# Optimization experiments

Hardware: AMD Instinct MI355X
Metric: run time of the kernel (lower is better)

Reference implementation:

```python
import jax, jax.numpy as jnp
import numpy as np
from jax.scipy.linalg import cho_solve

N = 4096        # num nodes
D = 256         # in_dim == out_dim
NUM_HOPS = 2
R = 32          # subspace_dim
ETA = 0.5
EPS_SUB = 0.5   # eps in coeff = r / (n * eps^2)
LN_EPS = 1e-5


def setup_inputs() -> dict:
    rng = np.random.default_rng(0)
    K = NUM_HOPS + 1
    # sparse-ish binary adjacency mask with self loops
    mask = (rng.random((N, N)) < 0.002).astype(np.float32)
    mask = np.maximum(mask, np.eye(N, dtype=np.float32))
    deg = mask.sum(axis=1, keepdims=True)
    A = (mask / deg).astype(np.float32)          # row-stochastic propagation
    L = (np.eye(N, dtype=np.float32) - A)        # normalized Laplacian
    H = rng.standard_normal((N, D)).astype(np.float32)
    # orthonormal subspace bases per hop, as in __init__ (QR of randn)
    U = np.stack([np.linalg.qr(rng.standard_normal((D, R)))[0][:, :R] for _ in range(K)]).astype(np.float32)
    lambda_laps = np.full((K,), 0.1, dtype=np.float32)
    hop_weights = np.full((K,), 1.0 / K, dtype=np.float32)
    threshold = np.full((D,), 0.05, dtype=np.float32)
    gamma = np.ones((D,), dtype=np.float32)
    beta = np.zeros((D,), dtype=np.float32)
    return {
        "H": jnp.asarray(H), "A": jnp.asarray(A), "adj_mask": jnp.asarray(mask),
        "L": jnp.asarray(L), "U": jnp.asarray(U),
        "lambda_laps": jnp.asarray(lambda_laps), "hop_weights": jnp.asarray(hop_weights),
        "threshold": jnp.asarray(threshold), "gamma": jnp.asarray(gamma), "beta": jnp.asarray(beta),
    }


def reference(H, A, adj_mask, L, U, lambda_laps, hop_weights, threshold, gamma, beta):
    n, d = H.shape
    r = U.shape[-1]
    # multi-hop propagation
    hops = [H]
    Hk = H
    for _ in range(NUM_HOPS):
        Hk = A @ Hk
        hops.append(Hk)
    w = jax.nn.softmax(hop_weights)
    laps = jax.nn.softplus(lambda_laps)
    coeff = r / (n * EPS_SUB ** 2)
    neg = (1.0 - adj_mask) * -1e9
    I_r = jnp.eye(r, dtype=H.dtype)
    agg = jnp.zeros_like(H)        # accumulates grad_k.T, shape [n, d]
    lap_total = jnp.zeros_like(H)
    for k, H_k in enumerate(hops):
        Uk = U[k]                  # [d, r]
        Zk = Uk.T @ H_k.T          # [r, n]
        M = I_r + coeff * (Zk @ Zk.T)              # [r, r], SPD
        Lc = jnp.linalg.cholesky(M)
        M_inv = cho_solve((Lc, True), I_r)         # cholesky_inverse
        MZ = M_inv @ Zk                            # [r, n]
        scores = Zk.T @ MZ + neg                   # [n, n] masked subspace attention
        alpha = jax.nn.softmax(scores, axis=1)
        grad_k = (Uk @ (MZ @ alpha.T)).T           # [n, d]
        agg = agg + w[k] * grad_k
        lap_total = lap_total + laps[k] * (L @ H_k)
    H_half = H + ETA * agg - ETA * lap_total
    # soft-threshold (proj is None since in_dim == out_dim)
    H_out = jnp.sign(H_half) * jax.nn.relu(jnp.abs(H_half) - threshold[None, :])
    H_out = H_out + H              # residual
    mu = H_out.mean(axis=-1, keepdims=True)
    var = H_out.var(axis=-1, keepdims=True)
    H_out = (H_out - mu) / jnp.sqrt(var + LN_EPS) * gamma + beta
    # orthogonality loss over all (k, l) pairs
    K = U.shape[0]
    orth_loss = jnp.asarray(0.0, dtype=H.dtype)
    for k in range(K):
        for l in range(k, K):
            G = U[k].T @ U[l]
            orth_loss = orth_loss + jnp.sum(((G - I_r) if l == k else G) ** 2)
    lap_smooth = jnp.sum(H_out * (L @ H_out))  # trace(H^T L H)
    return H_out, orth_loss, lap_smooth, jax.lax.stop_gradient(w)
```

## Files before the change

### kernel.cpp

```cpp
#include <hip/hip_runtime.h>
#include <math.h>

#define NN 4096
#define DD 256
#define KK 3
#define RR 32
#define MAXNNZ 128

static constexpr float ETA    = 0.5f;
static constexpr float COEFF  = 0.03125f;
static constexpr float LN_EPSF = 1e-5f;

#define OFF_H1   0
#define OFF_H2   (NN*DD)
#define OFF_H3   (2*NN*DD)
#define OFF_Y    (3*NN*DD)
#define OFF_P    (OFF_Y + KK*NN*RR)
#define OFF_M    (OFF_P + KK*NN*RR)
#define OFF_MINV (OFF_M + KK*RR*RR)
#define OFF_SCAL (OFF_MINV + KK*RR*RR)
#define OFF_NNZ  (OFF_SCAL + 8)
#define OFF_COLS (OFF_NNZ + NN)
#define OFF_VALS (OFF_COLS + NN*MAXNNZ)
#define OFF_PART (OFF_VALS + NN*MAXNNZ)
#define OFF_ORTH (OFF_PART + NN/4)
#define OFF_W    (OFF_ORTH + 8)

__global__ void k_csr_prep(const float* __restrict__ A, int* __restrict__ nnz,
                           int* __restrict__ cols, float* __restrict__ vals,
                           const float* __restrict__ hw, const float* __restrict__ ll,
                           const float* __restrict__ U,
                           float* __restrict__ ws, float* __restrict__ out) {
  int b = blockIdx.x;
  int t = threadIdx.x;
  if (b >= NN/4) {
    int p = b - NN/4;
    if (p == 6) {
      if (t == 0) {
        float m = fmaxf(fmaxf(hw[0], hw[1]), hw[2]);
        float e0 = expf(hw[0]-m), e1 = expf(hw[1]-m), e2 = expf(hw[2]-m);
        float s = e0 + e1 + e2;
        float w0 = e0/s, w1 = e1/s, w2 = e2/s;
        ws[OFF_SCAL+0] = w0; ws[OFF_SCAL+1] = w1; ws[OFF_SCAL+2] = w2;
        for (int k = 0; k < KK; ++k) {
          float x = ll[k];
          ws[OFF_SCAL+3+k] = (x > 20.f) ? x : log1pf(expf(x));
        }
        out[NN*DD + 2] = w0; out[NN*DD + 3] = w1; out[NN*DD + 4] = w2;
      }
      for (int idx = t; idx < KK*RR*RR; idx += 256) {
        int rr2 = idx % (RR*RR);
        ws[OFF_M + idx] = ((rr2 / RR) == (rr2 % RR)) ? 1.f : 0.f;
      }
      return;
    }
    int k = (p < 3) ? 0 : ((p < 5) ? 1 : 2);
    int l = (p < 3) ? p : ((p < 5) ? p - 2 : 2);
    int a0 = t >> 5, bb = t & 31;
    float s0 = 0.f, s1 = 0.f, s2 = 0.f, s3 = 0.f;
    for (int dd = 0; dd < DD; ++dd) {
      float ul = U[(size_t)l*DD*RR + dd*RR + bb];
      const float* uk = U + (size_t)k*DD*RR + dd*RR;
      s0 += uk[a0]      * ul;
      s1 += uk[a0 + 8]  * ul;
      s2 += uk[a0 + 16] * ul;
      s3 += uk[a0 + 24] * ul;
    }
    if (k == l && bb == a0)      s0 -= 1.f;
    if (k == l && bb == a0 + 8)  s1 -= 1.f;
    if (k == l && bb == a0 + 16) s2 -= 1.f;
    if (k == l && bb == a0 + 24) s3 -= 1.f;
    float sq = s0*s0 + s1*s1 + s2*s2 + s3*s3;
    #pragma unroll
    for (int o = 32; o > 0; o >>= 1) sq += __shfl_xor(sq, o, 64);
    __shared__ float red[4];
    if ((t & 63) == 0) red[t >> 6] = sq;
    __syncthreads();
    if (t == 0) ws[OFF_ORTH + p] = red[0] + red[1] + red[2] + red[3];
    return;
  }
  int w = t >> 6, lane = t & 63;
  int i = b * 4 + w;
  const float4* row4 = (const float4*)(A + (size_t)i * NN);
  float4 vv[16];
  #pragma unroll
  for (int it = 0; it < 16; ++it) vv[it] = row4[it*64 + lane];
  int* ci = cols + i*MAXNNZ;
  float* vi = vals + i*MAXNNZ;
  unsigned long long lower = lane ? (~0ull >> (64 - lane)) : 0ull;
  int base = 0;
  #pragma unroll
  for (int it = 0; it < 16; ++it) {
    float4 v = vv[it];
    int jb = (it*64 + lane) * 4;
    unsigned long long mx = __ballot(v.x != 0.f);
    unsigned long long my = __ballot(v.y != 0.f);
    unsigned long long mz = __ballot(v.z != 0.f);
    unsigned long long mw = __ballot(v.w != 0.f);
    int before = __popcll(mx & lower) + __popcll(my & lower)
               + __popcll(mz & lower) + __popcll(mw & lower);
    int p0 = base + before;
    int bx = (mx >> lane) & 1, by = (my >> lane) & 1, bz = (mz >> lane) & 1;
    if (v.x != 0.f && p0 < MAXNNZ)                    { ci[p0] = jb;   vi[p0] = v.x; }
    int p1 = p0 + bx;
    if (v.y != 0.f && p1 < MAXNNZ)                    { ci[p1] = jb+1; vi[p1] = v.y; }
    int p2 = p1 + by;
    if (v.z != 0.f && p2 < MAXNNZ)                    { ci[p2] = jb+2; vi[p2] = v.z; }
    int p3 = p2 + bz;
    if (v.w != 0.f && p3 < MAXNNZ)                    { ci[p3] = jb+3; vi[p3] = v.w; }
    base += __popcll(mx) + __popcll(my) + __popcll(mz) + __popcll(mw);
  }
  int n = base < MAXNNZ ? base : MAXNNZ;
  int npad = (n + 7) & ~7;
  for (int e = n + lane; e < npad; e += 64) {
    ci[e] = i;
    vi[e] = 0.f;
  }
  if (lane == 0) nnz[i] = n;
}

__device__ __forceinline__ void spmv_quad(const float* __restrict__ X, int row, int lane,
                                          const int* __restrict__ nnz,
                                          const int* __restrict__ cols,
                                          const float* __restrict__ vals,
                                          float4& acc, float4& own) {
  int d4 = lane * 4;
  int n = nnz[row];
  int npad = (n + 7) & ~7;
  const int* ci = cols + row*MAXNNZ;
  const float* vi = vals + row*MAXNNZ;
  for (int e0 = 0; e0 < npad; e0 += 8) {
    int4 c0 = *(const int4*)(ci + e0);
    int4 c1 = *(const int4*)(ci + e0 + 4);
    float4 v0 = *(const float4*)(vi + e0);
    float4 v1 = *(const float4*)(vi + e0 + 4);
    float4 x0 = *(const float4*)(X + (size_t)c0.x*DD + d4);
    float4 x1 = *(const float4*)(X + (size_t)c0.y*DD + d4);
    float4 x2 = *(const float4*)(X + (size_t)c0.z*DD + d4);
    float4 x3 = *(const float4*)(X + (size_t)c0.w*DD + d4);
    float4 x4 = *(const float4*)(X + (size_t)c1.x*DD + d4);
    float4 x5 = *(const float4*)(X + (size_t)c1.y*DD + d4);
    float4 x6 = *(const float4*)(X + (size_t)c1.z*DD + d4);
    float4 x7 = *(const float4*)(X + (size_t)c1.w*DD + d4);
    if (c0.x == row) own = x0;
    if (c0.y == row) own = x1;
    if (c0.z == row) own = x2;
    if (c0.w == row) own = x3;
    if (c1.x == row) own = x4;
    if (c1.y == row) own = x5;
    if (c1.z == row) own = x6;
    if (c1.w == row) own = x7;
    acc.x += v0.x*x0.x + v0.y*x1.x + v0.z*x2.x + v0.w*x3.x + v1.x*x4.x + v1.y*x5.x + v1.z*x6.x + v1.w*x7.x;
    acc.y += v0.x*x0.y + v0.y*x1.y + v0.z*x2.y + v0.w*x3.y + v1.x*x4.y + v1.y*x5.y + v1.z*x6.y + v1.w*x7.y;
    acc.z += v0.x*x0.z + v0.y*x1.z + v0.z*x2.z + v0.w*x3.z + v1.x*x4.z + v1.y*x5.z + v1.z*x6.z + v1.w*x7.z;
    acc.w += v0.x*x0.w + v0.y*x1.w + v0.z*x2.w + v0.w*x3.w + v1.x*x4.w + v1.y*x5.w + v1.z*x6.w + v1.w*x7.w;
  }
}

__global__ void k_spmvy(const float* __restrict__ X, float* __restrict__ Hout,
                        const int* __restrict__ nnz, const int* __restrict__ cols,
                        const float* __restrict__ vals,
                        const float* __restrict__ Uo, float* __restrict__ Yo,
                        const float* __restrict__ Un, float* __restrict__ Yn) {
  int t = threadIdx.x;
  int r = t >> 6, lane = t & 63;
  int row = blockIdx.x * 4 + r;
  int d4 = lane * 4;
  float4 acc = {0.f, 0.f, 0.f, 0.f};
  float4 own = {0.f, 0.f, 0.f, 0.f};
  spmv_quad(X, row, lane, nnz, cols, vals, acc, own);
  *(float4*)(Hout + (size_t)row*DD + d4) = acc;
  if (!Uo && !Un) return;
  __shared__ float Hs[4][2][DD];
  *(float4*)&Hs[r][0][d4] = own;
  *(float4*)&Hs[r][1][d4] = acc;
  __syncthreads();
  int c = lane & 31, h = lane >> 5;
  if (Uo) {
    float part = 0.f;
    #pragma unroll 8
    for (int d = h*128; d < h*128 + 128; ++d) part += Hs[r][0][d] * Uo[d*RR + c];
    part += __shfl_xor(part, 32, 64);
    if (h == 0) Yo[(size_t)row*RR + c] = part;
  }
  if (Un) {
    float part = 0.f;
    #pragma unroll 8
    for (int d = h*128; d < h*128 + 128; ++d) part += Hs[r][1][d] * Un[d*RR + c];
    part += __shfl_xor(part, 32, 64);
    if (h == 0) Yn[(size_t)row*RR + c] = part;
  }
}

__global__ __launch_bounds__(1024) void k_gram(const float* __restrict__ Y, float* __restrict__ M) {
  int k = blockIdx.y;
  __shared__ float Ys[128*RR];
  int t = threadIdx.x;
  const float* Yk = Y + (size_t)k*NN*RR + (size_t)blockIdx.x*128*RR;
  for (int idx = t; idx < 128*RR; idx += 1024) Ys[idx] = Yk[idx];
  __syncthreads();
  int a = t >> 5, b = t & 31;
  float s = 0.f;
  for (int i = 0; i < 128; ++i) s += Ys[i*RR + a] * Ys[i*RR + b];
  atomicAdd(&M[k*RR*RR + a*RR + b], COEFF * s);
}

__global__ __launch_bounds__(256) void k_gj(const float* __restrict__ M, float* __restrict__ Minv,
                                            const float* __restrict__ U, float* __restrict__ W) {
  int k = blockIdx.x;
  int g = blockIdx.y;
  int t = threadIdx.x;
  __shared__ float B[RR][2*RR + 1];
  for (int idx = t; idx < RR*2*RR; idx += 256) {
    int r = idx >> 6, c = idx & 63;
    B[r][c] = (c < RR) ? M[k*RR*RR + r*RR + c] : ((c - RR == r) ? 1.f : 0.f);
  }
  __syncthreads();
  if (t < 64) {
    for (int p = 0; p < RR; ++p) {
      float rd = 1.f / B[p][p];
      float pb = B[p][t] * rd;
      float f[RR];
      #pragma unroll
      for (int r = 0; r < RR; ++r) f[r] = B[r][p];
      B[p][t] = pb;
      #pragma unroll
      for (int r = 0; r < RR; ++r) {
        if (r == p) continue;
        B[r][t] -= f[r] * pb;
      }
    }
  }
  __syncthreads();
  if (g == 0)
    for (int idx = t; idx < RR*RR; idx += 256)
      Minv[k*RR*RR + idx] = B[idx >> 5][RR + (idx & 31)];
  for (int e = 0; e < 8; ++e) {
    int idx = t + e*256;
    int d = g*64 + (idx >> 5), rr2 = idx & 31;
    const float* ud = U + (size_t)k*DD*RR + (size_t)d*RR;
    float s = 0.f;
    #pragma unroll
    for (int a = 0; a < RR; ++a) s += ud[a] * B[a][RR + rr2];
    W[(size_t)k*DD*RR + (size_t)d*RR + rr2] = s;
  }
}

__global__ __launch_bounds__(256) void k_attn(const float* __restrict__ Y, const float* __restrict__ Minv,
                       float* __restrict__ P, const int* __restrict__ nnz,
                       const int* __restrict__ cols, const float* __restrict__ vals,
                       const float* __restrict__ H2, float* __restrict__ H3) {
  int k = blockIdx.y;
  int t = threadIdx.x;
  int w = t >> 6, lane = t & 63;
  if (blockIdx.x >= NN/4) {
    if (k != 0) return;
    int row = (blockIdx.x - NN/4) * 4 + w;
    float4 acc = {0.f, 0.f, 0.f, 0.f};
    float4 own;
    spmv_quad(H2, row, lane, nnz, cols, vals, acc, own);
    *(float4*)(H3 + (size_t)row*DD + lane*4) = acc;
    return;
  }
  int i = blockIdx.x * 4 + w;
  const float* Yk = Y + (size_t)k*NN*RR;
  __shared__ float Mi[RR*RR];
  __shared__ float Yi[4][RR];
  __shared__ float qv[4][RR];
  __shared__ float sc[4][MAXNNZ];
  __shared__ float Yc[4][32][RR + 1];
  for (int idx = t; idx < RR*RR; idx += 256) Mi[idx] = Minv[k*RR*RR + idx];
  if (lane < RR) Yi[w][lane] = Yk[(size_t)i*RR + lane];
  sc[w][lane] = -1e30f; sc[w][lane+64] = -1e30f;
  __syncthreads();
  if (lane < RR) {
    float s = 0.f;
    #pragma unroll 8
    for (int a = 0; a < RR; ++a) s += Mi[a*RR + lane] * Yi[w][a];
    qv[w][lane] = s;
  }
  int g = lane >> 2, a4 = lane & 3;
  const float* qq = &qv[w][8*a4];
  float q0 = qq[0], q1 = qq[1], q2 = qq[2], q3 = qq[3];
  float q4 = qq[4], q5 = qq[5], q6 = qq[6], q7 = qq[7];
  int n = nnz[i], npad = (n + 7) & ~7;
  const int* ci = cols + i*MAXNNZ;
  for (int e0 = 0; e0 < npad; e0 += 16) {
    int e = e0 + g;
    int ee = (e < npad) ? e : 0;
    int col = ci[ee];
    const float4* yr = (const float4*)(Yk + (size_t)col*RR + 8*a4);
    float4 y0 = yr[0], y1 = yr[1];
    if (e < 32) {
      *(float4*)&Yc[w][e][8*a4]     = y0;
      *(float4*)&Yc[w][e][8*a4 + 4] = y1;
    }
    float s = y0.x*q0 + y0.y*q1 + y0.z*q2 + y0.w*q3
            + y1.x*q4 + y1.y*q5 + y1.z*q6 + y1.w*q7;
    s += __shfl_xor(s, 1, 64);
    s += __shfl_xor(s, 2, 64);
    if (a4 == 0 && e < npad) sc[w][e] = (e < n) ? s : -1e30f;
  }
  float s0 = sc[w][lane], s1 = sc[w][lane+64];
  float m = fmaxf(s0, s1);
  #pragma unroll
  for (int o = 32; o > 0; o >>= 1) m = fmaxf(m, __shfl_xor(m, o, 64));
  float e0v = expf(s0 - m), e1v = expf(s1 - m);
  sc[w][lane] = e0v; sc[w][lane+64] = e1v;
  float l = e0v + e1v;
  #pragma unroll
  for (int o = 32; o > 0; o >>= 1) l += __shfl_xor(l, o, 64);
  float linv = 1.f / l;
  int c = lane & 31, h = lane >> 5;
  float acc = 0.f;
  int lim = npad < 32 ? npad : 32;
  for (int e = h; e < lim; e += 2) acc += sc[w][e] * Yc[w][e][c];
  for (int e = 32 + h; e < npad; e += 2) acc += sc[w][e] * Yk[(size_t)ci[e]*RR + c];
  acc += __shfl_xor(acc, 32, 64);
  if (lane < RR) P[(size_t)k*NN*RR + (size_t)i*RR + lane] = acc * linv;
}

__global__ void k_epi(const float* __restrict__ H0, const float* __restrict__ ws,
                      const float* __restrict__ thr,
                      const float* __restrict__ gma, const float* __restrict__ bta,
                      float* __restrict__ out) {
  __shared__ float Us[DD][RR+1];
  __shared__ float Ps[8][KK*RR];
  int t = threadIdx.x;
  int ty = t >> 5, tx = t & 31;
  int row0 = blockIdx.x * 8;
  const float* P    = ws + OFF_P;
  const float* scal = ws + OFF_SCAL;
  const float* W    = ws + OFF_W;
  for (int idx = t; idx < 8*KK*RR; idx += 256) {
    int rl = idx / (KK*RR), kr = idx % (KK*RR);
    int k = kr / RR, rr2 = kr % RR;
    Ps[rl][kr] = P[(size_t)k*NN*RR + (size_t)(row0+rl)*RR + rr2];
  }
  float lp0 = scal[3], lp1 = scal[4], lp2 = scal[5];
  float gacc[8];
  #pragma unroll
  for (int j = 0; j < 8; ++j) gacc[j] = 0.f;
  for (int k = 0; k < KK; ++k) {
    __syncthreads();
    for (int idx = t; idx < DD*RR/4; idx += 256) {
      float4 w4 = *(const float4*)(W + (size_t)k*DD*RR + (size_t)idx*4);
      int d = (idx*4) >> 5, c = (idx*4) & 31;
      Us[d][c] = w4.x; Us[d][c+1] = w4.y; Us[d][c+2] = w4.z; Us[d][c+3] = w4.w;
    }
    __syncthreads();
    float wk = scal[k];
    #pragma unroll
    for (int j = 0; j < 8; ++j) {
      int d = tx + 32*j;
      float s = 0.f;
      #pragma unroll
      for (int rr2 = 0; rr2 < RR; ++rr2) s += Ps[ty][k*RR + rr2] * Us[d][rr2];
      gacc[j] += wk * s;
    }
  }
  int i = row0 + ty;
  const float* H1 = ws + OFF_H1;
  const float* H2 = ws + OFF_H2;
  const float* H3 = ws + OFF_H3;
  float v[8]; float sum = 0.f, sumsq = 0.f;
  #pragma unroll
  for (int j = 0; j < 8; ++j) {
    int d = tx + 32*j;
    size_t idx = (size_t)i*DD + d;
    float h0 = H0[idx], h1 = H1[idx], h2 = H2[idx], h3 = H3[idx];
    float lap = lp0*(h0-h1) + lp1*(h1-h2) + lp2*(h2-h3);
    float hf = h0 + ETA*gacc[j] - ETA*lap;
    float a = fabsf(hf) - thr[d];
    float sft = (a > 0.f) ? copysignf(a, hf) : 0.f;
    float x = sft + h0;
    v[j] = x; sum += x; sumsq += x*x;
  }
  #pragma unroll
  for (int o = 16; o > 0; o >>= 1) {
    sum   += __shfl_xor(sum, o, 32);
    sumsq += __shfl_xor(sumsq, o, 32);
  }
  float mu  = sum * (1.f/DD);
  float var = sumsq * (1.f/DD) - mu*mu;
  float inv = rsqrtf(var + LN_EPSF);
  #pragma unroll
  for (int j = 0; j < 8; ++j) {
    int d = tx + 32*j;
    out[(size_t)i*DD + d] = (v[j] - mu) * inv * gma[d] + bta[d];
  }
}

__global__ void k_lapsm(const float* __restrict__ Hout, const int* __restrict__ nnz,
                        const int* __restrict__ cols, const float* __restrict__ vals,
                        float* __restrict__ partial) {
  int t = threadIdx.x;
  int row = blockIdx.x * 4 + (t >> 6);
  int d4 = (t & 63) * 4;
  int n = nnz[row];
  int npad = (n + 7) & ~7;
  const int* ci = cols + row*MAXNNZ;
  const float* vi = vals + row*MAXNNZ;
  float4 acc = {0.f, 0.f, 0.f, 0.f};
  for (int e0 = 0; e0 < npad; e0 += 8) {
    int4 c0 = *(const int4*)(ci + e0);
    int4 c1 = *(const int4*)(ci + e0 + 4);
    float4 v0 = *(const float4*)(vi + e0);
    float4 v1 = *(const float4*)(vi + e0 + 4);
    float4 x0 = *(const float4*)(Hout + (size_t)c0.x*DD + d4);
    float4 x1 = *(const float4*)(Hout + (size_t)c0.y*DD + d4);
    float4 x2 = *(const float4*)(Hout + (size_t)c0.z*DD + d4);
    float4 x3 = *(const float4*)(Hout + (size_t)c0.w*DD + d4);
    float4 x4 = *(const float4*)(Hout + (size_t)c1.x*DD + d4);
    float4 x5 = *(const float4*)(Hout + (size_t)c1.y*DD + d4);
    float4 x6 = *(const float4*)(Hout + (size_t)c1.z*DD + d4);
    float4 x7 = *(const float4*)(Hout + (size_t)c1.w*DD + d4);
    acc.x += v0.x*x0.x + v0.y*x1.x + v0.z*x2.x + v0.w*x3.x + v1.x*x4.x + v1.y*x5.x + v1.z*x6.x + v1.w*x7.x;
    acc.y += v0.x*x0.y + v0.y*x1.y + v0.z*x2.y + v0.w*x3.y + v1.x*x4.y + v1.y*x5.y + v1.z*x6.y + v1.w*x7.y;
    acc.z += v0.x*x0.z + v0.y*x1.z + v0.z*x2.z + v0.w*x3.z + v1.x*x4.z + v1.y*x5.z + v1.z*x6.z + v1.w*x7.z;
    acc.w += v0.x*x0.w + v0.y*x1.w + v0.z*x2.w + v0.w*x3.w + v1.x*x4.w + v1.y*x5.w + v1.z*x6.w + v1.w*x7.w;
  }
  float4 h = *(const float4*)(Hout + (size_t)row*DD + d4);
  float part = h.x*(h.x-acc.x) + h.y*(h.y-acc.y) + h.z*(h.z-acc.z) + h.w*(h.w-acc.w);
  #pragma unroll
  for (int o = 32; o > 0; o >>= 1) part += __shfl_xor(part, o, 64);
  __shared__ float red[4];
  if ((t & 63) == 0) red[t >> 6] = part;
  __syncthreads();
  if (t == 0) partial[blockIdx.x] = red[0] + red[1] + red[2] + red[3];
}

__global__ void k_red(const float* __restrict__ ws, float* __restrict__ out) {
  const float* partial = ws + OFF_PART;
  int t = threadIdx.x;
  float4 p = *(const float4*)(partial + t*4);
  float s = p.x + p.y + p.z + p.w;
  #pragma unroll
  for (int o = 32; o > 0; o >>= 1) s += __shfl_xor(s, o, 64);
  __shared__ float red[4];
  if ((t & 63) == 0) red[t >> 6] = s;
  __syncthreads();
  if (t == 0) {
    out[1] = red[0] + red[1] + red[2] + red[3];
    const float* op = ws + OFF_ORTH;
    out[0] = op[0] + op[1] + op[2] + op[3] + op[4] + op[5];
  }
}

extern "C" void kernel_launch(void* const* d_in, const int* in_sizes, int n_in,
                              void* d_out, int out_size, void* d_ws, size_t ws_size,
                              hipStream_t stream) {
  const float* H   = (const float*)d_in[0];
  const float* A   = (const float*)d_in[1];
  const float* U   = (const float*)d_in[4];
  const float* ll  = (const float*)d_in[5];
  const float* hw  = (const float*)d_in[6];
  const float* thr = (const float*)d_in[7];
  const float* gma = (const float*)d_in[8];
  const float* bta = (const float*)d_in[9];
  float* out = (float*)d_out;
  float* ws  = (float*)d_ws;
  int* nnz   = (int*)(ws + OFF_NNZ);
  int* cols  = (int*)(ws + OFF_COLS);
  float* vals = ws + OFF_VALS;
  float* Y = ws + OFF_Y;

  k_csr_prep<<<NN/4 + 7, 256, 0, stream>>>(A, nnz, cols, vals, hw, ll, U, ws, out);
  k_spmvy<<<NN/4, 256, 0, stream>>>(H, ws + OFF_H1, nnz, cols, vals,
                                    U, Y, U + (size_t)DD*RR, Y + (size_t)NN*RR);
  k_spmvy<<<NN/4, 256, 0, stream>>>(ws + OFF_H1, ws + OFF_H2, nnz, cols, vals,
                                    nullptr, nullptr, U + (size_t)2*DD*RR, Y + (size_t)2*NN*RR);
  dim3 g32(NN/128, KK);
  k_gram<<<g32, 1024, 0, stream>>>(Y, ws + OFF_M);
  dim3 ggj(KK, 4);
  k_gj<<<ggj, 256, 0, stream>>>(ws + OFF_M, ws + OFF_MINV, U, ws + OFF_W);
  dim3 gattn(NN/4 + NN/4, KK);
  k_attn<<<gattn, 256, 0, stream>>>(Y, ws + OFF_MINV, ws + OFF_P, nnz, cols, vals,
                                    ws + OFF_H2, ws + OFF_H3);
  k_epi<<<NN/8, 256, 0, stream>>>(H, ws, thr, gma, bta, out);
  k_lapsm<<<NN/4, 256, 0, stream>>>(out, nnz, cols, vals, ws + OFF_PART);
  k_red<<<1, 256, 0, stream>>>(ws, out + NN*DD);
}
```

Baseline: 290.0 us.

## Split dense-to-CSR row scan across two waves with shared-memory merge

Each adjacency row is now scanned by two wavefronts, each covering half the columns, instead of one wave per row. The compacted column indices and values go to shared memory, then are merged and written to global memory with coalesced stores. The grid doubles, and launch bounds are added so register use drops from 16 to 8 float4 loads per thread and more waves can be resident. This is meant to hide latency on the 64MB dense read of A, at the cost of a block-level sync and a shared-memory staging step.

```diff
diff --git a/kernel.cpp b/kernel.cpp
--- a/kernel.cpp
+++ b/kernel.cpp
@@ -26,15 +26,16 @@
 #define OFF_ORTH (OFF_PART + NN/4)
 #define OFF_W    (OFF_ORTH + 8)
 
-__global__ void k_csr_prep(const float* __restrict__ A, int* __restrict__ nnz,
-                           int* __restrict__ cols, float* __restrict__ vals,
-                           const float* __restrict__ hw, const float* __restrict__ ll,
-                           const float* __restrict__ U,
-                           float* __restrict__ ws, float* __restrict__ out) {
+__global__ __launch_bounds__(256, 8)
+void k_csr_prep(const float* __restrict__ A, int* __restrict__ nnz,
+                int* __restrict__ cols, float* __restrict__ vals,
+                const float* __restrict__ hw, const float* __restrict__ ll,
+                const float* __restrict__ U,
+                float* __restrict__ ws, float* __restrict__ out) {
   int b = blockIdx.x;
   int t = threadIdx.x;
-  if (b >= NN/4) {
-    int p = b - NN/4;
+  if (b >= NN/2) {
+    int p = b - NN/2;
     if (p == 6) {
       if (t == 0) {
         float m = fmaxf(fmaxf(hw[0], hw[1]), hw[2]);
@@ -80,19 +81,21 @@
     return;
   }
   int w = t >> 6, lane = t & 63;
-  int i = b * 4 + w;
+  int r = w >> 1, h2 = w & 1;
+  int i = b * 2 + r;
+  __shared__ int   cbuf[2][2][MAXNNZ];
+  __shared__ float vbuf[2][2][MAXNNZ];
+  __shared__ int   cnts[4];
   const float4* row4 = (const float4*)(A + (size_t)i * NN);
-  float4 vv[16];
-  #pragma unroll
-  for (int it = 0; it < 16; ++it) vv[it] = row4[it*64 + lane];
-  int* ci = cols + i*MAXNNZ;
-  float* vi = vals + i*MAXNNZ;
+  float4 vv[8];
+  #pragma unroll
+  for (int it = 0; it < 8; ++it) vv[it] = row4[h2*512 + it*64 + lane];
   unsigned long long lower = lane ? (~0ull >> (64 - lane)) : 0ull;
   int base = 0;
   #pragma unroll
-  for (int it = 0; it < 16; ++it) {
+  for (int it = 0; it < 8; ++it) {
     float4 v = vv[it];
-    int jb = (it*64 + lane) * 4;
+    int jb = (h2*512 + it*64 + lane) * 4;
     unsigned long long mx = __ballot(v.x != 0.f);
     unsigned long long my = __ballot(v.y != 0.f);
     unsigned long long mz = __ballot(v.z != 0.f);
@@ -101,22 +104,32 @@
                + __popcll(mz & lower) + __popcll(mw & lower);
     int p0 = base + before;
     int bx = (mx >> lane) & 1, by = (my >> lane) & 1, bz = (mz >> lane) & 1;
-    if (v.x != 0.f && p0 < MAXNNZ)                    { ci[p0] = jb;   vi[p0] = v.x; }
+    if (v.x != 0.f && p0 < MAXNNZ)  { cbuf[r][h2][p0] = jb;   vbuf[r][h2][p0] = v.x; }
     int p1 = p0 + bx;
-    if (v.y != 0.f && p1 < MAXNNZ)                    { ci[p1] = jb+1; vi[p1] = v.y; }
+    if (v.y != 0.f && p1 < MAXNNZ)  { cbuf[r][h2][p1] = jb+1; vbuf[r][h2][p1] = v.y; }
     int p2 = p1 + by;
-    if (v.z != 0.f && p2 < MAXNNZ)                    { ci[p2] = jb+2; vi[p2] = v.z; }
+    if (v.z != 0.f && p2 < MAXNNZ)  { cbuf[r][h2][p2] = jb+2; vbuf[r][h2][p2] = v.z; }
     int p3 = p2 + bz;
-    if (v.w != 0.f && p3 < MAXNNZ)                    { ci[p3] = jb+3; vi[p3] = v.w; }
+    if (v.w != 0.f && p3 < MAXNNZ)  { cbuf[r][h2][p3] = jb+3; vbuf[r][h2][p3] = v.w; }
     base += __popcll(mx) + __popcll(my) + __popcll(mz) + __popcll(mw);
   }
-  int n = base < MAXNNZ ? base : MAXNNZ;
+  if (lane == 0) cnts[w] = base < MAXNNZ ? base : MAXNNZ;
+  __syncthreads();
+  int rr = t >> 7, e0 = t & 127;
+  int ii = b * 2 + rr;
+  int n0 = cnts[rr*2], n1 = cnts[rr*2 + 1];
+  int n = n0 + n1; if (n > MAXNNZ) n = MAXNNZ;
   int npad = (n + 7) & ~7;
-  for (int e = n + lane; e < npad; e += 64) {
-    ci[e] = i;
-    vi[e] = 0.f;
-  }
-  if (lane == 0) nnz[i] = n;
+  for (int e = e0; e < npad; e += 128) {
+    int c; float v;
+    if (e < n) {
+      if (e < n0) { c = cbuf[rr][0][e];      v = vbuf[rr][0][e]; }
+      else        { c = cbuf[rr][1][e - n0]; v = vbuf[rr][1][e - n0]; }
+    } else { c = ii; v = 0.f; }
+    cols[ii*MAXNNZ + e] = c;
+    vals[ii*MAXNNZ + e] = v;
+  }
+  if (e0 == 0) nnz[ii] = n;
 }
 
 __device__ __forceinline__ void spmv_quad(const float* __restrict__ X, int row, int lane,
@@ -465,7 +478,7 @@
   float* vals = ws + OFF_VALS;
   float* Y = ws + OFF_Y;
 
-  k_csr_prep<<<NN/4 + 7, 256, 0, stream>>>(A, nnz, cols, vals, hw, ll, U, ws, out);
+  k_csr_prep<<<NN/2 + 7, 256, 0, stream>>>(A, nnz, cols, vals, hw, ll, U, ws, out);
   k_spmvy<<<NN/4, 256, 0, stream>>>(H, ws + OFF_H1, nnz, cols, vals,
                                     U, Y, U + (size_t)DD*RR, Y + (size_t)NN*RR);
   k_spmvy<<<NN/4, 256, 0, stream>>>(ws + OFF_H1, ws + OFF_H2, nnz, cols, vals,
```

After: 288.5 us. No clear change (-0.5%).
